# Performance work log

Hardware: AMD Instinct MI355X
Metric: run time of the kernel (lower is better)

## Reference

```python
import jax, jax.numpy as jnp
import numpy as np

N_NODES = 100000
N_EDGES = 1250000
D_FEAT = 64


def setup_inputs() -> dict:
    key = jax.random.key(0)
    k1, k2 = jax.random.split(key)
    x = jax.random.normal(k1, (N_NODES, D_FEAT), dtype=jnp.float32)
    edge_index = jax.random.randint(k2, (2, N_EDGES), 0, N_NODES, dtype=jnp.int64)
    return {"t": 0, "x": x, "edge_index": edge_index}


def reference(t, x, edge_index):
    # LGConv(normalize=False): out[i] = sum_{(j->i) in E} x[j]
    # adj_t SpMM expressed as gather + segment-sum scatter.
    src = edge_index[0]  # source/neighbor nodes
    dst = edge_index[1]  # destination nodes
    msgs = x[src]  # [E, D] gather
    out = jax.ops.segment_sum(msgs, dst, num_segments=N_NODES)  # [N, D]
    return out
```

## Files before the change

kernel.cpp:

```cpp
#include <hip/hip_runtime.h>

#define N_NODES 100000
#define N_EDGES 1250000
#define D_FEAT 64

#define NB_SHIFT 7
#define NODES_PER_B 128
#define N_BUCKETS ((N_NODES + NODES_PER_B - 1) / NODES_PER_B)
#define TROW (N_BUCKETS + 1)
#define NB_PAD 1024
#define MAX_BUCKET_EDGES 2048
#define SRC_BITS 17
#define SRC_MASK ((1u << SRC_BITS) - 1u)

#define CH 4992
#define NCH ((N_EDGES + CH - 1) / CH)
#define NCHP 256

#define QFEAT 16
#define QS_US4 (N_NODES * 4)
#define QS_US  (N_NODES * QFEAT)

typedef float f32x4 __attribute__((ext_vector_type(4)));

__global__ __launch_bounds__(256) void lgconv_scatter(
    const float* __restrict__ x, const int* __restrict__ src,
    const int* __restrict__ dst, float* __restrict__ out) {
    int tid  = blockIdx.x * blockDim.x + threadIdx.x;
    int edge = tid >> 4;
    int f4   = (tid & 15) << 2;
    if (edge >= N_EDGES) return;
    int s = src[edge], d = dst[edge];
    const float4 v = *reinterpret_cast<const float4*>(x + (size_t)s * D_FEAT + f4);
    float* o = out + (size_t)d * D_FEAT + f4;
    unsafeAtomicAdd(o + 0, v.x); unsafeAtomicAdd(o + 1, v.y);
    unsafeAtomicAdd(o + 2, v.z); unsafeAtomicAdd(o + 3, v.w);
}

__device__ __forceinline__ unsigned short f2bf(float f) {
    unsigned int u = __float_as_uint(f);
    return (unsigned short)((u + 0x7FFFu + ((u >> 16) & 1u)) >> 16);
}
__device__ __forceinline__ float bflo(unsigned int p) {
    return __uint_as_float(p << 16);
}
__device__ __forceinline__ float bfhi(unsigned int p) {
    return __uint_as_float(p & 0xFFFF0000u);
}

__device__ __forceinline__ int wscan_incl(int v) {
    const int lane = threadIdx.x & 63;
#pragma unroll
    for (int off = 1; off < 64; off <<= 1) {
        int u = __shfl_up(v, off, 64);
        if (lane >= off) v += u;
    }
    return v;
}

template <bool CONV>
__global__ __launch_bounds__(1024) void k1_sort(
    const float* __restrict__ x, unsigned short* __restrict__ xb,
    const int* __restrict__ src, const int* __restrict__ dst,
    unsigned int* __restrict__ bins, unsigned short* __restrict__ tableT) {
    __shared__ int hist[NB_PAD];
    __shared__ int scanBase[NB_PAD];
    __shared__ int cur[NB_PAD];
    __shared__ int wsum[16];
    __shared__ unsigned int stage[CH];
    const int t    = threadIdx.x;
    const int c    = blockIdx.x;
    const int base = c * CH;
    const int cnt  = min(CH, N_EDGES - base);
    const int lane = t & 63;
    const int wid  = t >> 6;

    if (CONV) {
        const int F4 = N_NODES * D_FEAT / 4;
        for (int i = c * 1024 + t; i < F4; i += NCH * 1024) {
            float4 v = reinterpret_cast<const float4*>(x)[i];
            ushort4 o;
            o.x = f2bf(v.x); o.y = f2bf(v.y); o.z = f2bf(v.z); o.w = f2bf(v.w);
            int node = i >> 4, j = i & 15;
            int q = j >> 2, w = j & 3;
            reinterpret_cast<ushort4*>(xb)[(size_t)q * QS_US4 + node * 4 + w] = o;
        }
    }

    hist[t] = 0; cur[t] = 0;
    __syncthreads();
    for (int i = t; i < cnt; i += 1024)
        atomicAdd(&hist[dst[base + i] >> NB_SHIFT], 1);
    __syncthreads();

    int v = hist[t];
    int s = wscan_incl(v);
    if (lane == 63) wsum[wid] = s;
    __syncthreads();
    if (t < 16) {
        int w  = wsum[t];
        wsum[t] = wscan_incl(w);
    }
    __syncthreads();
    int incl = s + (wid ? wsum[wid - 1] : 0);
    scanBase[t] = incl - v;
    __syncthreads();

    if (t < TROW) tableT[(size_t)t * NCHP + c] = (unsigned short)scanBase[t];

    for (int i = t; i < cnt; i += 1024) {
        int d = dst[base + i], sv = src[base + i];
        int b = d >> NB_SHIFT;
        unsigned int packed = ((unsigned int)(d & (NODES_PER_B - 1)) << SRC_BITS)
                            | (unsigned int)sv;
        int pos = scanBase[b] + atomicAdd(&cur[b], 1);
        stage[pos] = packed;
    }
    __syncthreads();
    for (int i = t; i < cnt; i += 1024) bins[base + i] = stage[i];
}

template <bool BF>
__global__ __launch_bounds__(512) void k2_accum(
    const float* __restrict__ x, const unsigned short* __restrict__ xb,
    const unsigned int* __restrict__ bins, const unsigned short* __restrict__ tableT,
    float* __restrict__ out) {
    __shared__ int            startA[512];
    __shared__ unsigned short lenA[512];
    __shared__ int            destB[512];
    __shared__ unsigned int   raw[MAX_BUCKET_EDGES];
    __shared__ unsigned int   srcs[MAX_BUCKET_EDGES];
    __shared__ int cntArr[NODES_PER_B];
    __shared__ int nodeOff[NODES_PER_B + 1];
    __shared__ int curN[NODES_PER_B];
    __shared__ int wsum[8];
    const int t    = threadIdx.x;
    const int b    = blockIdx.x;
    const int lane = t & 63;
    const int wid  = t >> 6;

    int st = 0, len = 0;
    if (t < NCH) {
        st  = __builtin_nontemporal_load(tableT + (size_t)b * NCHP + t);
        len = (int)__builtin_nontemporal_load(tableT + (size_t)(b + 1) * NCHP + t) - st;
    }
    startA[t] = st;
    lenA[t]   = (unsigned short)len;
    if (t < NODES_PER_B) cntArr[t] = 0;
    int s = wscan_incl(len);
    if (lane == 63) wsum[wid] = s;
    __syncthreads();
    if (t < 8) {
        int w  = wsum[t];
        wsum[t] = wscan_incl(w);
    }
    __syncthreads();
    int incl = s + (wid ? wsum[wid - 1] : 0);
    destB[t] = incl - len;
    int cntTot = wsum[7];
    if (cntTot > MAX_BUCKET_EDGES) cntTot = MAX_BUCKET_EDGES;
    __syncthreads();

    {
        const int cj = t >> 3;
        const int jj = t & 7;
        for (int c0 = 0; c0 < NCH; c0 += 64) {
            int c = c0 + cj;
            if (c < NCH) {
                int l = lenA[c], s0 = startA[c], db = destB[c];
                const unsigned int* p = bins + (size_t)c * CH + s0;
                for (int q = jj; q < l; q += 8)
                    raw[db + q] = __builtin_nontemporal_load(p + q);
            }
        }
    }
    __syncthreads();

    for (int i = t; i < cntTot; i += 512)
        atomicAdd(&cntArr[raw[i] >> SRC_BITS], 1);
    __syncthreads();
    int v2 = (t < NODES_PER_B) ? cntArr[t] : 0;
    int s2 = wscan_incl(v2);
    if (t < NODES_PER_B && lane == 63) wsum[wid] = s2;
    __syncthreads();
    if (t < NODES_PER_B) {
        int excl = s2 + ((wid == 1) ? wsum[0] : 0) - v2;
        nodeOff[t] = excl;
        curN[t]    = excl;
    }
    if (t == 0) nodeOff[NODES_PER_B] = cntTot;
    __syncthreads();
    for (int i = t; i < cntTot; i += 512) {
        unsigned int p = raw[i];
        int pos = atomicAdd(&curN[p >> SRC_BITS], 1);
        srcs[pos] = p & SRC_MASK;
    }
    __syncthreads();

    if (BF) {
        const int fl  = t & 1;
        const int grp = (t >> 1) & 3;
        const int sub = t >> 3;
        for (int q = 0; q < 4; ++q) {
            const unsigned short* xq = xb + (size_t)q * QS_US;
            for (int g = 0; g < 2; ++g) {
                int local = g * 64 + sub;
                int node  = b * NODES_PER_B + local;
                int beg = nodeOff[local], end = nodeOff[local + 1];
                float a0=0,a1=0,a2=0,a3=0,a4=0,a5=0,a6=0,a7=0;
                int k = beg + grp;
                for (; k + 4 < end; k += 8) {
                    const uint4 u0 = *reinterpret_cast<const uint4*>(
                        xq + (size_t)srcs[k] * QFEAT + fl * 8);
                    const uint4 u1 = *reinterpret_cast<const uint4*>(
                        xq + (size_t)srcs[k + 4] * QFEAT + fl * 8);
                    a0 += bflo(u0.x) + bflo(u1.x);
                    a1 += bfhi(u0.x) + bfhi(u1.x);
                    a2 += bflo(u0.y) + bflo(u1.y);
                    a3 += bfhi(u0.y) + bfhi(u1.y);
                    a4 += bflo(u0.z) + bflo(u1.z);
                    a5 += bfhi(u0.z) + bfhi(u1.z);
                    a6 += bflo(u0.w) + bflo(u1.w);
                    a7 += bfhi(u0.w) + bfhi(u1.w);
                }
                for (; k < end; k += 4) {
                    const uint4 u = *reinterpret_cast<const uint4*>(
                        xq + (size_t)srcs[k] * QFEAT + fl * 8);
                    a0 += bflo(u.x); a1 += bfhi(u.x);
                    a2 += bflo(u.y); a3 += bfhi(u.y);
                    a4 += bflo(u.z); a5 += bfhi(u.z);
                    a6 += bflo(u.w); a7 += bfhi(u.w);
                }
                a0 += __shfl_xor(a0, 2, 64); a1 += __shfl_xor(a1, 2, 64);
                a2 += __shfl_xor(a2, 2, 64); a3 += __shfl_xor(a3, 2, 64);
                a4 += __shfl_xor(a4, 2, 64); a5 += __shfl_xor(a5, 2, 64);
                a6 += __shfl_xor(a6, 2, 64); a7 += __shfl_xor(a7, 2, 64);
                a0 += __shfl_xor(a0, 4, 64); a1 += __shfl_xor(a1, 4, 64);
                a2 += __shfl_xor(a2, 4, 64); a3 += __shfl_xor(a3, 4, 64);
                a4 += __shfl_xor(a4, 4, 64); a5 += __shfl_xor(a5, 4, 64);
                a6 += __shfl_xor(a6, 4, 64); a7 += __shfl_xor(a7, 4, 64);
                if (grp == 0 && node < N_NODES) {
                    float* op = out + (size_t)node * D_FEAT + q * QFEAT + fl * 8;
                    f32x4 w0 = {a0, a1, a2, a3};
                    f32x4 w1 = {a4, a5, a6, a7};
                    __builtin_nontemporal_store(w0, reinterpret_cast<f32x4*>(op));
                    __builtin_nontemporal_store(w1, reinterpret_cast<f32x4*>(op + 4));
                }
            }
            __syncthreads();
        }
    } else {
        int lane4 = (t & 15) << 2;
        for (int g = 0; g < NODES_PER_B / 32; ++g) {
            int local = g * 32 + (t >> 4);
            int node  = b * NODES_PER_B + local;
            int beg = nodeOff[local], end = nodeOff[local + 1];
            float4 acc = make_float4(0.f, 0.f, 0.f, 0.f);
            int k = beg;
            for (; k + 1 < end; k += 2) {
                unsigned int i0 = srcs[k], i1 = srcs[k + 1];
                const float4 a = *reinterpret_cast<const float4*>(x + (size_t)i0 * D_FEAT + lane4);
                const float4 c = *reinterpret_cast<const float4*>(x + (size_t)i1 * D_FEAT + lane4);
                acc.x += a.x + c.x; acc.y += a.y + c.y;
                acc.z += a.z + c.z; acc.w += a.w + c.w;
            }
            if (k < end) {
                unsigned int i0 = srcs[k];
                const float4 a = *reinterpret_cast<const float4*>(x + (size_t)i0 * D_FEAT + lane4);
                acc.x += a.x; acc.y += a.y; acc.z += a.z; acc.w += a.w;
            }
            if (node < N_NODES)
                *reinterpret_cast<float4*>(out + (size_t)node * D_FEAT + lane4) = acc;
        }
    }
}

extern "C" void kernel_launch(void* const* d_in, const int* in_sizes, int n_in,
                              void* d_out, int out_size, void* d_ws, size_t ws_size,
                              hipStream_t stream) {
    const float* x   = (const float*)d_in[1];
    const int*   ei  = (const int*)d_in[2];
    const int*   src = ei;
    const int*   dst = ei + N_EDGES;
    float*       out = (float*)d_out;

    const size_t tabBytes = (size_t)TROW * NCHP * sizeof(unsigned short);
    const size_t binBytes = (size_t)N_EDGES * sizeof(unsigned int);
    const size_t xbOff    = (binBytes + tabBytes + 15) & ~(size_t)15;
    const size_t needA    = xbOff + (size_t)N_NODES * D_FEAT * sizeof(unsigned short);
    const size_t needB    = binBytes + tabBytes;

    if (ws_size >= needA) {
        unsigned int*   bins   = (unsigned int*)d_ws;
        unsigned short* tableT = (unsigned short*)((char*)d_ws + binBytes);
        unsigned short* xb     = (unsigned short*)((char*)d_ws + xbOff);
        k1_sort<true><<<NCH, 1024, 0, stream>>>(x, xb, src, dst, bins, tableT);
        k2_accum<true><<<N_BUCKETS, 512, 0, stream>>>(x, xb, bins, tableT, out);
    } else if (ws_size >= needB) {
        unsigned int*   bins   = (unsigned int*)d_ws;
        unsigned short* tableT = (unsigned short*)((char*)d_ws + binBytes);
        k1_sort<false><<<NCH, 1024, 0, stream>>>(x, nullptr, src, dst, bins, tableT);
        k2_accum<false><<<N_BUCKETS, 512, 0, stream>>>(x, nullptr, bins, tableT, out);
    } else {
        (void)hipMemsetAsync(out, 0, (size_t)out_size * sizeof(float), stream);
        const int total = N_EDGES * 16;
        lgconv_scatter<<<(total + 255) / 256, 256, 0, stream>>>(x, src, dst, out);
    }
}
```

Measured before the change: 140.8 us.

## Sort bucket edges by source range and gather full bf16 rows per node

Keeps the bf16 copy of x in row-major order instead of four feature-quarter planes. Within each destination bucket, edges are now sorted by (dst node, source range of 25000 nodes), so all blocks sweep the same source range in step, separated by block barriers. The aim is better L2 locality on the gathered rows. Each node's 64 features are now handled by 8 lanes, each holding two nodes' accumulators, which removes the cross-lane shuffle reduction. The costs are a larger 512-key scan and more registers per thread.

```diff
diff --git a/kernel.cpp b/kernel.cpp
--- a/kernel.cpp
+++ b/kernel.cpp
@@ -17,9 +17,9 @@
 #define NCH ((N_EDGES + CH - 1) / CH)
 #define NCHP 256
 
-#define QFEAT 16
-#define QS_US4 (N_NODES * 4)
-#define QS_US  (N_NODES * QFEAT)
+#define NR 4
+#define RANGE_SZ 25000u
+#define NKEY (NODES_PER_B * NR)
 
 typedef float f32x4 __attribute__((ext_vector_type(4)));
 
@@ -81,9 +81,7 @@
             float4 v = reinterpret_cast<const float4*>(x)[i];
             ushort4 o;
             o.x = f2bf(v.x); o.y = f2bf(v.y); o.z = f2bf(v.z); o.w = f2bf(v.w);
-            int node = i >> 4, j = i & 15;
-            int q = j >> 2, w = j & 3;
-            reinterpret_cast<ushort4*>(xb)[(size_t)q * QS_US4 + node * 4 + w] = o;
+            reinterpret_cast<ushort4*>(xb)[i] = o;
         }
     }
 
@@ -130,9 +128,9 @@
     __shared__ int            destB[512];
     __shared__ unsigned int   raw[MAX_BUCKET_EDGES];
     __shared__ unsigned int   srcs[MAX_BUCKET_EDGES];
-    __shared__ int cntArr[NODES_PER_B];
-    __shared__ int nodeOff[NODES_PER_B + 1];
-    __shared__ int curN[NODES_PER_B];
+    __shared__ int cntArr[NKEY];
+    __shared__ int nodeOff[NKEY + 1];
+    __shared__ int curN[NKEY];
     __shared__ int wsum[8];
     const int t    = threadIdx.x;
     const int b    = blockIdx.x;
@@ -146,7 +144,7 @@
     }
     startA[t] = st;
     lenA[t]   = (unsigned short)len;
-    if (t < NODES_PER_B) cntArr[t] = 0;
+    cntArr[t] = 0;
     int s = wscan_incl(len);
     if (lane == 63) wsum[wid] = s;
     __syncthreads();
@@ -176,44 +174,48 @@
     }
     __syncthreads();
 
-    for (int i = t; i < cntTot; i += 512)
-        atomicAdd(&cntArr[raw[i] >> SRC_BITS], 1);
-    __syncthreads();
-    int v2 = (t < NODES_PER_B) ? cntArr[t] : 0;
-    int s2 = wscan_incl(v2);
-    if (t < NODES_PER_B && lane == 63) wsum[wid] = s2;
-    __syncthreads();
-    if (t < NODES_PER_B) {
-        int excl = s2 + ((wid == 1) ? wsum[0] : 0) - v2;
-        nodeOff[t] = excl;
-        curN[t]    = excl;
-    }
-    if (t == 0) nodeOff[NODES_PER_B] = cntTot;
-    __syncthreads();
     for (int i = t; i < cntTot; i += 512) {
         unsigned int p = raw[i];
-        int pos = atomicAdd(&curN[p >> SRC_BITS], 1);
+        int key = ((p >> SRC_BITS) << 2) | ((p & SRC_MASK) / RANGE_SZ);
+        atomicAdd(&cntArr[key], 1);
+    }
+    __syncthreads();
+    int v2 = cntArr[t];
+    int s2 = wscan_incl(v2);
+    if (lane == 63) wsum[wid] = s2;
+    __syncthreads();
+    if (t < 8) {
+        int w  = wsum[t];
+        wsum[t] = wscan_incl(w);
+    }
+    __syncthreads();
+    int excl = s2 + (wid ? wsum[wid - 1] : 0) - v2;
+    nodeOff[t] = excl;
+    curN[t]    = excl;
+    if (t == 0) nodeOff[NKEY] = cntTot;
+    __syncthreads();
+    for (int i = t; i < cntTot; i += 512) {
+        unsigned int p = raw[i];
+        int key = ((p >> SRC_BITS) << 2) | ((p & SRC_MASK) / RANGE_SZ);
+        int pos = atomicAdd(&curN[key], 1);
         srcs[pos] = p & SRC_MASK;
     }
     __syncthreads();
 
     if (BF) {
-        const int fl  = t & 1;
-        const int grp = (t >> 1) & 3;
+        const int f0  = (t & 7) << 3;
         const int sub = t >> 3;
-        for (int q = 0; q < 4; ++q) {
-            const unsigned short* xq = xb + (size_t)q * QS_US;
-            for (int g = 0; g < 2; ++g) {
-                int local = g * 64 + sub;
-                int node  = b * NODES_PER_B + local;
-                int beg = nodeOff[local], end = nodeOff[local + 1];
-                float a0=0,a1=0,a2=0,a3=0,a4=0,a5=0,a6=0,a7=0;
-                int k = beg + grp;
-                for (; k + 4 < end; k += 8) {
+        float a0=0,a1=0,a2=0,a3=0,a4=0,a5=0,a6=0,a7=0;
+        float b0=0,b1=0,b2=0,b3=0,b4=0,b5=0,b6=0,b7=0;
+        for (int r = 0; r < NR; ++r) {
+            {
+                int idx = (sub << 2) | r;
+                int k = nodeOff[idx], end = nodeOff[idx + 1];
+                for (; k + 1 < end; k += 2) {
                     const uint4 u0 = *reinterpret_cast<const uint4*>(
-                        xq + (size_t)srcs[k] * QFEAT + fl * 8);
+                        xb + (size_t)srcs[k] * D_FEAT + f0);
                     const uint4 u1 = *reinterpret_cast<const uint4*>(
-                        xq + (size_t)srcs[k + 4] * QFEAT + fl * 8);
+                        xb + (size_t)srcs[k + 1] * D_FEAT + f0);
                     a0 += bflo(u0.x) + bflo(u1.x);
                     a1 += bfhi(u0.x) + bfhi(u1.x);
                     a2 += bflo(u0.y) + bflo(u1.y);
@@ -223,38 +225,67 @@
                     a6 += bflo(u0.w) + bflo(u1.w);
                     a7 += bfhi(u0.w) + bfhi(u1.w);
                 }
-                for (; k < end; k += 4) {
+                if (k < end) {
                     const uint4 u = *reinterpret_cast<const uint4*>(
-                        xq + (size_t)srcs[k] * QFEAT + fl * 8);
+                        xb + (size_t)srcs[k] * D_FEAT + f0);
                     a0 += bflo(u.x); a1 += bfhi(u.x);
                     a2 += bflo(u.y); a3 += bfhi(u.y);
                     a4 += bflo(u.z); a5 += bfhi(u.z);
                     a6 += bflo(u.w); a7 += bfhi(u.w);
                 }
-                a0 += __shfl_xor(a0, 2, 64); a1 += __shfl_xor(a1, 2, 64);
-                a2 += __shfl_xor(a2, 2, 64); a3 += __shfl_xor(a3, 2, 64);
-                a4 += __shfl_xor(a4, 2, 64); a5 += __shfl_xor(a5, 2, 64);
-                a6 += __shfl_xor(a6, 2, 64); a7 += __shfl_xor(a7, 2, 64);
-                a0 += __shfl_xor(a0, 4, 64); a1 += __shfl_xor(a1, 4, 64);
-                a2 += __shfl_xor(a2, 4, 64); a3 += __shfl_xor(a3, 4, 64);
-                a4 += __shfl_xor(a4, 4, 64); a5 += __shfl_xor(a5, 4, 64);
-                a6 += __shfl_xor(a6, 4, 64); a7 += __shfl_xor(a7, 4, 64);
-                if (grp == 0 && node < N_NODES) {
-                    float* op = out + (size_t)node * D_FEAT + q * QFEAT + fl * 8;
-                    f32x4 w0 = {a0, a1, a2, a3};
-                    f32x4 w1 = {a4, a5, a6, a7};
-                    __builtin_nontemporal_store(w0, reinterpret_cast<f32x4*>(op));
-                    __builtin_nontemporal_store(w1, reinterpret_cast<f32x4*>(op + 4));
+            }
+            {
+                int idx = ((64 + sub) << 2) | r;
+                int k = nodeOff[idx], end = nodeOff[idx + 1];
+                for (; k + 1 < end; k += 2) {
+                    const uint4 u0 = *reinterpret_cast<const uint4*>(
+                        xb + (size_t)srcs[k] * D_FEAT + f0);
+                    const uint4 u1 = *reinterpret_cast<const uint4*>(
+                        xb + (size_t)srcs[k + 1] * D_FEAT + f0);
+                    b0 += bflo(u0.x) + bflo(u1.x);
+                    b1 += bfhi(u0.x) + bfhi(u1.x);
+                    b2 += bflo(u0.y) + bflo(u1.y);
+                    b3 += bfhi(u0.y) + bfhi(u1.y);
+                    b4 += bflo(u0.z) + bflo(u1.z);
+                    b5 += bfhi(u0.z) + bfhi(u1.z);
+                    b6 += bflo(u0.w) + bflo(u1.w);
+                    b7 += bfhi(u0.w) + bfhi(u1.w);
                 }
+                if (k < end) {
+                    const uint4 u = *reinterpret_cast<const uint4*>(
+                        xb + (size_t)srcs[k] * D_FEAT + f0);
+                    b0 += bflo(u.x); b1 += bfhi(u.x);
+                    b2 += bflo(u.y); b3 += bfhi(u.y);
+                    b4 += bflo(u.z); b5 += bfhi(u.z);
+                    b6 += bflo(u.w); b7 += bfhi(u.w);
+                }
             }
             __syncthreads();
+        }
+        {
+            int node = b * NODES_PER_B + sub;
+            if (node < N_NODES) {
+                float* op = out + (size_t)node * D_FEAT + f0;
+                f32x4 w0 = {a0, a1, a2, a3};
+                f32x4 w1 = {a4, a5, a6, a7};
+                __builtin_nontemporal_store(w0, reinterpret_cast<f32x4*>(op));
+                __builtin_nontemporal_store(w1, reinterpret_cast<f32x4*>(op + 4));
+            }
+            node = b * NODES_PER_B + 64 + sub;
+            if (node < N_NODES) {
+                float* op = out + (size_t)node * D_FEAT + f0;
+                f32x4 w0 = {b0, b1, b2, b3};
+                f32x4 w1 = {b4, b5, b6, b7};
+                __builtin_nontemporal_store(w0, reinterpret_cast<f32x4*>(op));
+                __builtin_nontemporal_store(w1, reinterpret_cast<f32x4*>(op + 4));
+            }
         }
     } else {
         int lane4 = (t & 15) << 2;
         for (int g = 0; g < NODES_PER_B / 32; ++g) {
             int local = g * 32 + (t >> 4);
             int node  = b * NODES_PER_B + local;
-            int beg = nodeOff[local], end = nodeOff[local + 1];
+            int beg = nodeOff[local << 2], end = nodeOff[(local << 2) + 4];
             float4 acc = make_float4(0.f, 0.f, 0.f, 0.f);
             int k = beg;
             for (; k + 1 < end; k += 2) {
```

Result: faster. 123.9 us (-12.0%).
